# Optimization experiments

Hardware: AMD Instinct MI355X
Metric: run time of the kernel (lower is better)

Reference implementation:

```python
import jax, jax.numpy as jnp
import numpy as np

KSIZE = 5
# OpenCV: sigma=0 -> sigma = 0.3*((ksize-1)*0.5 - 1) + 0.8
SIGMA = 0.3 * ((KSIZE - 1) * 0.5 - 1.0) + 0.8  # = 1.1 for ksize=5


def _gauss_taps(ksize, sigma):
    r = (ksize - 1) / 2.0
    xs = np.arange(ksize, dtype=np.float64) - r
    w = np.exp(-(xs ** 2) / (2.0 * sigma ** 2))
    w /= w.sum()
    return jnp.asarray(w, dtype=jnp.float32)


def setup_inputs() -> dict:
    key = jax.random.key(0)
    x = jax.random.normal(key, (64, 384, 512, 3), dtype=jnp.float32)
    return {"x": x}


def reference(x):
    # Separable 5x5 Gaussian blur, OpenCV default border BORDER_REFLECT_101
    # (numpy/jnp 'reflect' mode, edge pixel not repeated).
    w = _gauss_taps(KSIZE, SIGMA)  # [5]
    pad = KSIZE // 2
    B, H, W, C = x.shape
    # vertical pass
    xp = jnp.pad(x, ((0, 0), (pad, pad), (0, 0), (0, 0)), mode="reflect")
    y = sum(w[k] * xp[:, k:k + H, :, :] for k in range(KSIZE))
    # horizontal pass
    yp = jnp.pad(y, ((0, 0), (0, 0), (pad, pad), (0, 0)), mode="reflect")
    out = sum(w[k] * yp[:, :, k:k + W, :] for k in range(KSIZE))
    return out
```

## Files before the change

kernel.cpp:

```cpp
#include <hip/hip_runtime.h>


#define BN 64
#define HN 384
#define WN 512
#define CN 3
#define ROWF (WN * CN)
#define ROWQ (ROWF / 4)
#define TH 4
#define NTILES (HN / TH)
#define NT 384

#define CW0 0.07076630f
#define CW1 0.24446040f
#define CW2 0.36954650f

__global__ __launch_bounds__(NT, 8) void gauss_blur_fused(
        const float* __restrict__ x, float* __restrict__ out) {
    __shared__ float v[TH * ROWF];

    const int tile = blockIdx.x;
    const int b    = tile / NTILES;
    const int h0   = (tile - b * NTILES) * TH;
    const float* __restrict__ xb = x + (size_t)b * HN * ROWF;
    float* __restrict__ ob = out + (size_t)b * HN * ROWF + (size_t)h0 * ROWF;

    const int q = threadIdx.x;

    float4 rowv[TH + 4];
#pragma unroll
    for (int i = 0; i < TH + 4; ++i) {
        int hs = h0 + i - 2;
        hs = hs < 0 ? -hs : hs;
        hs = hs >= HN ? 2 * HN - 2 - hs : hs;
        rowv[i] = ((const float4*)(xb + (size_t)hs * ROWF))[q];
    }
#pragma unroll
    for (int r = 0; r < TH; ++r) {
        float4 a;
        a.x = CW0 * (rowv[r].x + rowv[r + 4].x) +
              CW1 * (rowv[r + 1].x + rowv[r + 3].x) + CW2 * rowv[r + 2].x;
        a.y = CW0 * (rowv[r].y + rowv[r + 4].y) +
              CW1 * (rowv[r + 1].y + rowv[r + 3].y) + CW2 * rowv[r + 2].y;
        a.z = CW0 * (rowv[r].z + rowv[r + 4].z) +
              CW1 * (rowv[r + 1].z + rowv[r + 3].z) + CW2 * rowv[r + 2].z;
        a.w = CW0 * (rowv[r].w + rowv[r + 4].w) +
              CW1 * (rowv[r + 1].w + rowv[r + 3].w) + CW2 * rowv[r + 2].w;
        ((float4*)v)[r * ROWQ + q] = a;
    }
    __syncthreads();

    if (q >= 2 && q < ROWQ - 2) {
#pragma unroll
        for (int r = 0; r < TH; ++r) {
            const float* vr = v + r * ROWF;
            float wnd[20];
#pragma unroll
            for (int j = 0; j < 5; ++j) {
                float4 t = ((const float4*)vr)[q - 2 + j];
                wnd[4 * j + 0] = t.x;
                wnd[4 * j + 1] = t.y;
                wnd[4 * j + 2] = t.z;
                wnd[4 * j + 3] = t.w;
            }
            float4 res;
#pragma unroll
            for (int j = 0; j < 4; ++j) {
                ((float*)&res)[j] =
                    CW0 * (wnd[j + 2] + wnd[j + 14]) +
                    CW1 * (wnd[j + 5] + wnd[j + 11]) +
                    CW2 * wnd[j + 8];
            }
            ((float4*)ob)[r * ROWQ + q] = res;
        }
    } else {
#pragma unroll
        for (int r = 0; r < TH; ++r) {
            const float* vr = v + r * ROWF;
            float4 res;
#pragma unroll
            for (int j = 0; j < 4; ++j) {
                int e  = 4 * q + j;
                int wp = e / 3;
                int c  = e - wp * 3;
                float s = 0.f;
#pragma unroll
                for (int k = 0; k < 5; ++k) {
                    int ws = wp + k - 2;
                    ws = ws < 0 ? -ws : ws;
                    ws = ws >= WN ? 2 * WN - 2 - ws : ws;
                    float wk = (k == 2) ? CW2 : ((k == 1 || k == 3) ? CW1 : CW0);
                    s += wk * vr[ws * 3 + c];
                }
                ((float*)&res)[j] = s;
            }
            ((float4*)ob)[r * ROWQ + q] = res;
        }
    }
}

extern "C" void kernel_launch(void* const* d_in, const int* in_sizes, int n_in,
                              void* d_out, int out_size, void* d_ws, size_t ws_size,
                              hipStream_t stream) {
    const float* x = (const float*)d_in[0];
    float* out = (float*)d_out;
    gauss_blur_fused<<<dim3(BN * NTILES), dim3(NT), 0, stream>>>(x, out);
}
```

Measured before the change: 265.1 us.

## Pad shared rows with reflected halos, remap blocks, and use nontemporal stores

Each shared-memory row gets two float4s of padding on each side, filled with reflect-101 halo values by a small group of threads, so every thread runs the same branch-free horizontal pass. Block IDs are remapped in an interleaved pattern across eight groups, probably to spread work across XCDs or L2 slices. Output writes use nontemporal stores to avoid polluting the cache, and the launch-bounds occupancy hint drops from 8 to 6. The cost is an extra __syncthreads and a slightly larger shared buffer.

```diff
diff --git a/kernel.cpp b/kernel.cpp
--- a/kernel.cpp
+++ b/kernel.cpp
@@ -10,16 +10,24 @@
 #define TH 4
 #define NTILES (HN / TH)
 #define NT 384
+#define NBLK (BN * NTILES)
+
+#define PADQ 2
+#define LROWQ (ROWQ + 2 * PADQ)
+#define LROWF (LROWQ * 4)
 
 #define CW0 0.07076630f
 #define CW1 0.24446040f
 #define CW2 0.36954650f
 
-__global__ __launch_bounds__(NT, 8) void gauss_blur_fused(
+typedef float vfloat4 __attribute__((ext_vector_type(4)));
+
+__global__ __launch_bounds__(NT, 6) void gauss_blur_fused(
         const float* __restrict__ x, float* __restrict__ out) {
-    __shared__ float v[TH * ROWF];
+    __shared__ float v[TH * LROWF];
 
-    const int tile = blockIdx.x;
+    const int bid  = blockIdx.x;
+    const int tile = (bid & 7) * (NBLK >> 3) + (bid >> 3);
     const int b    = tile / NTILES;
     const int h0   = (tile - b * NTILES) * TH;
     const float* __restrict__ xb = x + (size_t)b * HN * ROWF;
@@ -46,56 +54,48 @@
               CW1 * (rowv[r + 1].z + rowv[r + 3].z) + CW2 * rowv[r + 2].z;
         a.w = CW0 * (rowv[r].w + rowv[r + 4].w) +
               CW1 * (rowv[r + 1].w + rowv[r + 3].w) + CW2 * rowv[r + 2].w;
-        ((float4*)v)[r * ROWQ + q] = a;
+        ((float4*)(v + r * LROWF))[PADQ + q] = a;
     }
     __syncthreads();
 
-    if (q >= 2 && q < ROWQ - 2) {
+    if (threadIdx.x < TH * 12) {
+        int r = threadIdx.x / 12;
+        int p = threadIdx.x - r * 12;
+        float* vr = v + r * LROWF + 4 * PADQ;
+        int dst, src;
+        if (p < 6) {
+            dst = p - 6;
+            src = (p < 3) ? 6 + p : p;
+        } else {
+            int pp = p - 6;
+            dst = 1536 + pp;
+            src = (pp < 3) ? 1530 + pp : 1524 + pp;
+        }
+        vr[dst] = vr[src];
+    }
+    __syncthreads();
+
 #pragma unroll
-        for (int r = 0; r < TH; ++r) {
-            const float* vr = v + r * ROWF;
-            float wnd[20];
+    for (int r = 0; r < TH; ++r) {
+        const float* vr = v + r * LROWF;
+        float wnd[20];
 #pragma unroll
-            for (int j = 0; j < 5; ++j) {
-                float4 t = ((const float4*)vr)[q - 2 + j];
-                wnd[4 * j + 0] = t.x;
-                wnd[4 * j + 1] = t.y;
-                wnd[4 * j + 2] = t.z;
-                wnd[4 * j + 3] = t.w;
-            }
-            float4 res;
+        for (int j = 0; j < 5; ++j) {
+            float4 t = ((const float4*)vr)[q + j];
+            wnd[4 * j + 0] = t.x;
+            wnd[4 * j + 1] = t.y;
+            wnd[4 * j + 2] = t.z;
+            wnd[4 * j + 3] = t.w;
+        }
+        vfloat4 res;
 #pragma unroll
-            for (int j = 0; j < 4; ++j) {
-                ((float*)&res)[j] =
-                    CW0 * (wnd[j + 2] + wnd[j + 14]) +
-                    CW1 * (wnd[j + 5] + wnd[j + 11]) +
-                    CW2 * wnd[j + 8];
-            }
-            ((float4*)ob)[r * ROWQ + q] = res;
+        for (int j = 0; j < 4; ++j) {
+            res[j] =
+                CW0 * (wnd[j + 2] + wnd[j + 14]) +
+                CW1 * (wnd[j + 5] + wnd[j + 11]) +
+                CW2 * wnd[j + 8];
         }
-    } else {
-#pragma unroll
-        for (int r = 0; r < TH; ++r) {
-            const float* vr = v + r * ROWF;
-            float4 res;
-#pragma unroll
-            for (int j = 0; j < 4; ++j) {
-                int e  = 4 * q + j;
-                int wp = e / 3;
-                int c  = e - wp * 3;
-                float s = 0.f;
-#pragma unroll
-                for (int k = 0; k < 5; ++k) {
-                    int ws = wp + k - 2;
-                    ws = ws < 0 ? -ws : ws;
-                    ws = ws >= WN ? 2 * WN - 2 - ws : ws;
-                    float wk = (k == 2) ? CW2 : ((k == 1 || k == 3) ? CW1 : CW0);
-                    s += wk * vr[ws * 3 + c];
-                }
-                ((float*)&res)[j] = s;
-            }
-            ((float4*)ob)[r * ROWQ + q] = res;
-        }
+        __builtin_nontemporal_store(res, &((vfloat4*)ob)[r * ROWQ + q]);
     }
 }
 
@@ -104,5 +104,5 @@
                               hipStream_t stream) {
     const float* x = (const float*)d_in[0];
     float* out = (float*)d_out;
-    gauss_blur_fused<<<dim3(BN * NTILES), dim3(NT), 0, stream>>>(x, out);
+    gauss_blur_fused<<<dim3(NBLK), dim3(NT), 0, stream>>>(x, out);
 }
```

Result: faster. 258.3 us (-2.6%).
